# Optimization experiments

Hardware: AMD Instinct MI355X
Metric: run time of the kernel (lower is better)

The kernel has to match this reference:

```python
import jax, jax.numpy as jnp
import numpy as np

B, N, NF, H = 16, 128, 128, 128


def setup_inputs() -> dict:
    key = jax.random.key(0)
    ks = jax.random.split(key, 10)
    s = lambda k, sh: jax.random.normal(k, sh, dtype=jnp.float32) * (1.0 / np.sqrt(sh[0]))
    return {
        "node_feat": jax.random.normal(ks[0], (B, N, NF), dtype=jnp.float32),
        "pos": jax.random.normal(ks[1], (B, N, 3), dtype=jnp.float32),
        "valid": jnp.ones((B, N), dtype=jnp.float32),
        "adj": jax.random.uniform(ks[2], (B, N, N), dtype=jnp.float32),
        "We1": s(ks[3], (2 * NF + 2, H)),
        "We2": s(ks[4], (H, H)),
        "Wc1": s(ks[5], (H, H)),
        "Wc2": s(ks[6], (H, 1)),
        "Wn1": s(ks[7], (NF + H, H)),
        "Wn2": s(ks[8], (H, NF)),
        "Wi": s(ks[9], (H, 1)),
    }


def reference(node_feat, pos, valid, adj, We1, We2, Wc1, Wc2, Wn1, Wn2, Wi):
    silu = jax.nn.silu
    n = node_feat.shape[1]
    # all-pairs broadcast features [B,N,N,NF]
    hi = jnp.broadcast_to(node_feat[:, :, None, :], (B, n, n, NF))
    hj = jnp.broadcast_to(node_feat[:, None, :, :], (B, n, n, NF))
    vec = pos[:, :, None, :] - pos[:, None, :, :]            # [B,N,N,3]
    dist = jnp.sum(vec * vec, axis=-1, keepdims=True)        # [B,N,N,1]
    adj4 = adj[..., None]                                    # [B,N,N,1]
    edge_input = jnp.concatenate([hi, hj, dist, adj4], axis=-1)
    m_ij = silu(silu(edge_input @ We1) @ We2)                # [B,N,N,H]
    # normalized direction vectors
    norm = jnp.linalg.norm(vec, axis=-1, keepdims=True)
    vecn = vec / jnp.maximum(norm, 1e-10)
    # pairwise valid mask [B,N,N,1]
    vmask = (valid[:, :, None] * valid[:, None, :])[..., None]
    # coordinate update
    C = (1.0 / (jnp.sum(valid, axis=-1) - 1.0))[:, None, None]
    phi_x = silu(m_ij @ Wc1) @ Wc2                           # [B,N,N,1]
    pos_new = pos + C * jnp.sum(vecn * phi_x * vmask, axis=2)
    # inference gating
    e_ij = jax.nn.sigmoid(m_ij @ Wi)
    m_ij = m_ij * e_ij
    # masked message aggregation over j
    message = jnp.sum(m_ij * adj4, axis=2)                   # [B,N,H]
    node_input = jnp.concatenate([node_feat, message], axis=-1)
    node_new = node_feat + silu(node_input @ Wn1) @ Wn2
    return node_new, pos_new
```

## Files before the change

kernel.cpp:

```cpp
#include <hip/hip_runtime.h>
#include <hip/hip_bf16.h>

#define B_  16
#define N_  128
#define NF_ 128
#define H_  128

typedef __attribute__((ext_vector_type(8))) short short8;
typedef __attribute__((ext_vector_type(4))) float floatx4;

__device__ __forceinline__ float silu_f(float x) {
    return x * __builtin_amdgcn_rcpf(1.0f + __expf(-x));
}
__device__ __forceinline__ float sigm_f(float x) {
    return __builtin_amdgcn_rcpf(1.0f + __expf(-x));
}
__device__ __forceinline__ unsigned short f2bf(float x) {
    union { float f; unsigned u; } v; v.f = x;
    unsigned r = (v.u + 0x7FFFu + ((v.u >> 16) & 1u)) >> 16;
    return (unsigned short)r;
}
__device__ __forceinline__ short f2bf_fast(float x) {
    union { __hip_bfloat16 h; short s; } u;
    u.h = __float2bfloat16(x);
    return u.s;
}
__device__ __forceinline__ float bf2f(unsigned short s) {
    union { unsigned u; float f; } v; v.u = ((unsigned)s) << 16;
    return v.f;
}
__device__ __forceinline__ int swz(int row, int k) {
    return row * 256 + ((((k >> 3) ^ (row & 15)) << 4) | ((k & 7) << 1));
}

__global__ __launch_bounds__(128) void k1_pre(const float* __restrict__ nf,
                                              const float* __restrict__ We1,
                                              float* __restrict__ A_ws,
                                              float* __restrict__ Bm_ws) {
    const int b  = blockIdx.x >> 4;
    const int r0 = (blockIdx.x & 15) << 3;
    const int h  = threadIdx.x;
    __shared__ float rows[8][128];
#pragma unroll
    for (int r = 0; r < 8; ++r)
        rows[r][h] = nf[((size_t)(b * N_ + r0 + r)) * NF_ + h];
    __syncthreads();
    float a[8], bm[8];
#pragma unroll
    for (int r = 0; r < 8; ++r) { a[r] = 0.f; bm[r] = 0.f; }
    for (int c = 0; c < NF_; ++c) {
        const float w1 = We1[c * H_ + h];
        const float w2 = We1[(NF_ + c) * H_ + h];
#pragma unroll
        for (int r = 0; r < 8; ++r) {
            const float x = rows[r][c];
            a[r]  = fmaf(x, w1, a[r]);
            bm[r] = fmaf(x, w2, bm[r]);
        }
    }
#pragma unroll
    for (int r = 0; r < 8; ++r) {
        A_ws [((size_t)(b * N_ + r0 + r)) * H_ + h] = a[r];
        Bm_ws[((size_t)(b * N_ + r0 + r)) * H_ + h] = bm[r];
    }
}

__global__ __launch_bounds__(64) void kC(const float* __restrict__ valid,
                                         float* __restrict__ Cinv) {
    const int b = blockIdx.x;
    const int t = threadIdx.x;
    float v = valid[b * N_ + t] + valid[b * N_ + 64 + t];
#pragma unroll
    for (int m = 32; m >= 1; m >>= 1) v += __shfl_down(v, m, 64);
    if (t == 0) Cinv[b] = 1.0f / (v - 1.0f);
}

#define OFF_BM    0
#define OFF_W2T   32768
#define OFF_WC1X  65536
#define OFF_MB    102400
#define OFF_AW    135168
#define OFF_WAB   139264
#define OFF_WC2   140288
#define OFF_POSJ  140800
#define OFF_VALJ  142336
#define OFF_POSI  142848
#define OFF_VALI  142976
#define SMEM_K2   143040

__global__ __launch_bounds__(512, 2) void k2_edge(
        const float* __restrict__ pos,
        const float* __restrict__ valid,
        const float* __restrict__ adj,
        const float* __restrict__ We1,
        const float* __restrict__ We2,
        const float* __restrict__ Wc1,
        const float* __restrict__ Wc2,
        const float* __restrict__ Wi,
        const float* __restrict__ A_ws,
        const float* __restrict__ Bm_ws,
        const float* __restrict__ Cinv,
        float* __restrict__ msg_ws,
        float* __restrict__ pos_out) {
    __shared__ __align__(16) char smem[SMEM_K2];
    char* BMb   = smem + OFF_BM;
    char* W2Tb  = smem + OFF_W2T;
    char* WC1Xb = smem + OFF_WC1X;
    char* MBb   = smem + OFF_MB;
    float* AWf  = (float*)(smem + OFF_AW);
    float* WABf = (float*)(smem + OFF_WAB);
    float* wc2s = (float*)(smem + OFF_WC2);
    float* posj = (float*)(smem + OFF_POSJ);
    float* valj = (float*)(smem + OFF_VALJ);
    float* posi = (float*)(smem + OFF_POSI);
    float* vali = (float*)(smem + OFF_VALI);

    const int tid = threadIdx.x;
    const int b   = blockIdx.x >> 4;
    const int i0  = (blockIdx.x & 15) << 3;

    for (int q = tid; q < (N_ * H_) / 4; q += 512) {
        const int j  = q >> 5;
        const int ch = (q << 2) & 127;
        const float4 v = *(const float4*)(Bm_ws + ((size_t)(b * N_ + j)) * H_ + ch);
        ushort4 o;
        o.x = f2bf(v.x); o.y = f2bf(v.y); o.z = f2bf(v.z); o.w = f2bf(v.w);
        *(ushort4*)(BMb + swz(j, ch)) = o;
    }
    for (int x = tid; x < H_ * H_; x += 512) {
        const int k = x >> 7, n = x & 127;
        *(unsigned short*)(W2Tb + swz(n, k)) = f2bf(We2[x]);
    }
    for (int x = tid; x < H_ * H_; x += 512) {
        const int k = x >> 7, n = x & 127;
        *(unsigned short*)(WC1Xb + swz(n, k)) = f2bf(Wc1[x]);
    }
    if (tid < 128)
        *(unsigned short*)(WC1Xb + swz(128, tid)) = f2bf(Wi[tid]);
    for (int x = tid; x < 15 * 128; x += 512)
        ((unsigned short*)(WC1Xb + 129 * 256))[x] = 0;
    for (int x = tid; x < 8 * H_; x += 512)
        AWf[x] = A_ws[((size_t)(b * N_ + i0)) * H_ + x];
    if (tid < 256) WABf[tid] = We1[256 * H_ + tid];
    if (tid < 128) {
        wc2s[tid] = Wc2[tid];
        valj[tid] = valid[b * N_ + tid];
    }
    if (tid >= 128) posj[tid - 128] = pos[b * N_ * 3 + (tid - 128)];
    if (tid < 24)   posi[tid] = pos[b * N_ * 3 + i0 * 3 + tid];
    if (tid >= 32 && tid < 40) vali[tid - 32] = valid[b * N_ + i0 + (tid - 32)];
    __syncthreads();

    const int w  = tid >> 6;
    const int l  = tid & 63;
    const int lr = l & 15;
    const int lg = l >> 4;
    const int i  = i0 + w;
    char* MBw = MBb + w * 4096;

    int csx[4];
#pragma unroll
    for (int ks = 0; ks < 4; ++ks) csx[ks] = ((ks * 4 + lg) ^ lr) << 4;

    float wc2v[8];
#pragma unroll
    for (int nt = 0; nt < 8; ++nt) wc2v[nt] = wc2s[nt * 16 + lr];
    const float vi   = vali[w];
    const float pix  = posi[w * 3 + 0], piy = posi[w * 3 + 1], piz = posi[w * 3 + 2];
    const float cinv = Cinv[b];

    float msg[8] = {0.f, 0.f, 0.f, 0.f, 0.f, 0.f, 0.f, 0.f};
    float px = 0.f, py = 0.f, pz = 0.f;
    const floatx4 zf = {0.f, 0.f, 0.f, 0.f};

    for (int jp = 0; jp < 4; ++jp) {
        const int j0 = jp * 32;
        float adjv[2], vmv[2], dst[2], vnx[2], vny[2], vnz[2];
#pragma unroll
        for (int c = 0; c < 2; ++c) {
            const int jj = j0 + c * 16 + lr;
            adjv[c] = adj[((size_t)(b * N_ + i)) * N_ + jj];
            const float vj = valj[jj];
            const float vx = pix - posj[jj * 3 + 0];
            const float vy = piy - posj[jj * 3 + 1];
            const float vz = piz - posj[jj * 3 + 2];
            dst[c] = vx * vx + vy * vy + vz * vz;
            vmv[c] = vi * vj;
            const float rn = __builtin_amdgcn_rcpf(fmaxf(sqrtf(dst[c]), 1e-10f));
            vnx[c] = vx * rn; vny[c] = vy * rn; vnz[c] = vz * rn;
        }

        short8 af[2][4];
#pragma unroll
        for (int c = 0; c < 2; ++c) {
            const int jj = j0 + c * 16 + lr;
#pragma unroll
            for (int ks = 0; ks < 4; ++ks) {
                const int co = ks * 32 + lg * 8;
                const short8 bm8 = *(const short8*)(BMb + jj * 256 + csx[ks]);
                const floatx4 a0 = *(const floatx4*)(AWf + w * 128 + co);
                const floatx4 a1 = *(const floatx4*)(AWf + w * 128 + co + 4);
                const floatx4 wa0 = *(const floatx4*)(WABf + co);
                const floatx4 wa1 = *(const floatx4*)(WABf + co + 4);
                const floatx4 wb0 = *(const floatx4*)(WABf + 128 + co);
                const floatx4 wb1 = *(const floatx4*)(WABf + 128 + co + 4);
#pragma unroll
                for (int e = 0; e < 8; ++e) {
                    const float aw = (e < 4) ? a0[e & 3] : a1[e & 3];
                    const float wa = (e < 4) ? wa0[e & 3] : wa1[e & 3];
                    const float wb = (e < 4) ? wb0[e & 3] : wb1[e & 3];
                    const float pre = aw + bf2f((unsigned short)bm8[e])
                                    + dst[c] * wa + adjv[c] * wb;
                    af[c][ks][e] = f2bf_fast(silu_f(pre));
                }
            }
        }

        floatx4 acc1[2][8];
#pragma unroll
        for (int c = 0; c < 2; ++c)
#pragma unroll
            for (int nt = 0; nt < 8; ++nt) acc1[c][nt] = zf;
#pragma unroll
        for (int nt = 0; nt < 8; ++nt)
#pragma unroll
            for (int ks = 0; ks < 4; ++ks) {
                const short8 bf = *(const short8*)(W2Tb + (nt * 16 + lr) * 256 + csx[ks]);
                acc1[0][nt] = __builtin_amdgcn_mfma_f32_16x16x32_bf16(af[0][ks], bf, acc1[0][nt], 0, 0, 0);
                acc1[1][nt] = __builtin_amdgcn_mfma_f32_16x16x32_bf16(af[1][ks], bf, acc1[1][nt], 0, 0, 0);
            }
#pragma unroll
        for (int c = 0; c < 2; ++c)
#pragma unroll
            for (int nt = 0; nt < 8; ++nt)
#pragma unroll
                for (int r = 0; r < 4; ++r)
                    acc1[c][nt][r] = silu_f(acc1[c][nt][r]);

        short8 af2[2][4];
#pragma unroll
        for (int c = 0; c < 2; ++c) {
#pragma unroll
            for (int nt = 0; nt < 8; ++nt)
#pragma unroll
                for (int r = 0; r < 4; ++r)
                    *(unsigned short*)(MBw + swz(lg * 4 + r, nt * 16 + lr)) =
                        (unsigned short)f2bf_fast(acc1[c][nt][r]);
#pragma unroll
            for (int ks = 0; ks < 4; ++ks)
                af2[c][ks] = *(const short8*)(MBw + lr * 256 + csx[ks]);
        }

        floatx4 accg[2];
        accg[0] = zf; accg[1] = zf;
#pragma unroll
        for (int ks = 0; ks < 4; ++ks) {
            const short8 bf = *(const short8*)(WC1Xb + (128 + lr) * 256 + csx[ks]);
            accg[0] = __builtin_amdgcn_mfma_f32_16x16x32_bf16(af2[0][ks], bf, accg[0], 0, 0, 0);
            accg[1] = __builtin_amdgcn_mfma_f32_16x16x32_bf16(af2[1][ks], bf, accg[1], 0, 0, 0);
        }
#pragma unroll
        for (int c = 0; c < 2; ++c) {
            float t4[4];
#pragma unroll
            for (int r = 0; r < 4; ++r) {
                const float ep  = __shfl(accg[c][r], l & 48);
                const float ajr = __shfl(adjv[c], (l & 48) | (lg * 4 + r));
                t4[r] = sigm_f(ep) * ajr;
            }
#pragma unroll
            for (int nt = 0; nt < 8; ++nt)
                msg[nt] += acc1[c][nt][0] * t4[0] + acc1[c][nt][1] * t4[1]
                         + acc1[c][nt][2] * t4[2] + acc1[c][nt][3] * t4[3];
        }

        float ph[2][4] = {{0.f, 0.f, 0.f, 0.f}, {0.f, 0.f, 0.f, 0.f}};
#pragma unroll
        for (int nt = 0; nt < 8; ++nt) {
            floatx4 acc2a = zf, acc2b = zf;
#pragma unroll
            for (int ks = 0; ks < 4; ++ks) {
                const short8 bf = *(const short8*)(WC1Xb + (nt * 16 + lr) * 256 + csx[ks]);
                acc2a = __builtin_amdgcn_mfma_f32_16x16x32_bf16(af2[0][ks], bf, acc2a, 0, 0, 0);
                acc2b = __builtin_amdgcn_mfma_f32_16x16x32_bf16(af2[1][ks], bf, acc2b, 0, 0, 0);
            }
            const float wv = wc2v[nt];
#pragma unroll
            for (int r = 0; r < 4; ++r) {
                ph[0][r] = fmaf(silu_f(acc2a[r]), wv, ph[0][r]);
                ph[1][r] = fmaf(silu_f(acc2b[r]), wv, ph[1][r]);
            }
        }
#pragma unroll
        for (int msk = 1; msk <= 8; msk <<= 1)
#pragma unroll
            for (int c = 0; c < 2; ++c)
#pragma unroll
                for (int r = 0; r < 4; ++r)
                    ph[c][r] += __shfl_xor(ph[c][r], msk);
        const int src = ((lr >> 2) << 4) | lr;
        const int rr  = lr & 3;
#pragma unroll
        for (int c = 0; c < 2; ++c) {
            const float q0 = __shfl(ph[c][0], src), q1 = __shfl(ph[c][1], src);
            const float q2 = __shfl(ph[c][2], src), q3 = __shfl(ph[c][3], src);
            const float phl = rr == 0 ? q0 : rr == 1 ? q1 : rr == 2 ? q2 : q3;
            const float pm = phl * vmv[c];
            px = fmaf(vnx[c], pm, px); py = fmaf(vny[c], pm, py); pz = fmaf(vnz[c], pm, pz);
        }
    }

#pragma unroll
    for (int msk = 16; msk <= 32; msk <<= 1)
#pragma unroll
        for (int nt = 0; nt < 8; ++nt)
            msg[nt] += __shfl_xor(msg[nt], msk);
    if (l < 16) {
#pragma unroll
        for (int nt = 0; nt < 8; ++nt)
            msg_ws[((size_t)(b * N_ + i)) * H_ + nt * 16 + l] = msg[nt];
    }
#pragma unroll
    for (int msk = 1; msk <= 8; msk <<= 1) {
        px += __shfl_xor(px, msk);
        py += __shfl_xor(py, msk);
        pz += __shfl_xor(pz, msk);
    }
    if (l == 0) {
        const size_t o = ((size_t)(b * N_ + i)) * 3;
        pos_out[o + 0] = pos[o + 0] + cinv * px;
        pos_out[o + 1] = pos[o + 1] + cinv * py;
        pos_out[o + 2] = pos[o + 2] + cinv * pz;
    }
}

__global__ __launch_bounds__(128) void k3_node(
        const float* __restrict__ nf,
        const float* __restrict__ Wn1,
        const float* __restrict__ Wn2,
        const float* __restrict__ msg_ws,
        float* __restrict__ out) {
    const int b  = blockIdx.x >> 4;
    const int r0 = (blockIdx.x & 15) << 3;
    const int h  = threadIdx.x;
    __shared__ float in_s[8][256];
    __shared__ float t_s[8][128];
#pragma unroll
    for (int r = 0; r < 8; ++r) {
        in_s[r][h]       = nf[((size_t)(b * N_ + r0 + r)) * NF_ + h];
        in_s[r][128 + h] = msg_ws[((size_t)(b * N_ + r0 + r)) * H_ + h];
    }
    __syncthreads();
    float acc[8];
#pragma unroll
    for (int r = 0; r < 8; ++r) acc[r] = 0.f;
    for (int c = 0; c < 256; ++c) {
        const float wv = Wn1[c * H_ + h];
#pragma unroll
        for (int r = 0; r < 8; ++r) acc[r] = fmaf(in_s[r][c], wv, acc[r]);
    }
#pragma unroll
    for (int r = 0; r < 8; ++r) t_s[r][h] = silu_f(acc[r]);
    __syncthreads();
    float o[8];
#pragma unroll
    for (int r = 0; r < 8; ++r) o[r] = 0.f;
    for (int c = 0; c < 128; ++c) {
        const float wv = Wn2[c * NF_ + h];
#pragma unroll
        for (int r = 0; r < 8; ++r) o[r] = fmaf(t_s[r][c], wv, o[r]);
    }
#pragma unroll
    for (int r = 0; r < 8; ++r)
        out[((size_t)(b * N_ + r0 + r)) * NF_ + h] = in_s[r][h] + o[r];
}

extern "C" void kernel_launch(void* const* d_in, const int* in_sizes, int n_in,
                              void* d_out, int out_size, void* d_ws, size_t ws_size,
                              hipStream_t stream) {
    const float* node_feat = (const float*)d_in[0];
    const float* pos   = (const float*)d_in[1];
    const float* valid = (const float*)d_in[2];
    const float* adj   = (const float*)d_in[3];
    const float* We1   = (const float*)d_in[4];
    const float* We2   = (const float*)d_in[5];
    const float* Wc1   = (const float*)d_in[6];
    const float* Wc2   = (const float*)d_in[7];
    const float* Wn1   = (const float*)d_in[8];
    const float* Wn2   = (const float*)d_in[9];
    const float* Wi    = (const float*)d_in[10];

    float* out     = (float*)d_out;
    float* pos_out = out + (size_t)B_ * N_ * NF_;

    const size_t node_elems = (size_t)B_ * N_ * H_;
    if (ws_size < (3 * node_elems + B_) * sizeof(float)) return;
    float* A_ws   = (float*)d_ws;
    float* Bm_ws  = A_ws + node_elems;
    float* msg_ws = Bm_ws + node_elems;
    float* Cinv   = msg_ws + node_elems;

    k1_pre<<<B_ * 16, 128, 0, stream>>>(node_feat, We1, A_ws, Bm_ws);
    kC<<<B_, 64, 0, stream>>>(valid, Cinv);
    k2_edge<<<B_ * 16, 512, 0, stream>>>(pos, valid, adj, We1, We2, Wc1, Wc2, Wi,
                                         A_ws, Bm_ws, Cinv, msg_ws, pos_out);
    k3_node<<<B_ * 16, 128, 0, stream>>>(node_feat, Wn1, Wn2, msg_ws, out);
}
```

Before: 78.92 us.

## Transpose edge MFMA output to feed next GEMM from registers, drop LDS staging

The first edge GEMM now computes the transposed product, with weights as the A operand. Its silu'd accumulator fragments can then be converted to bf16 and used directly as B operands of 16x16x16 bf16 MFMAs for the gating and coordinate GEMMs. This removes the per-wave LDS write/read round trip for the intermediate m_ij tile and about 32KB of shared memory. The epilogue reductions for the gate, phi and message are reworked to match the transposed layout. In exchange it issues twice as many smaller-K MFMAs, and relies on the 16x16x16 instruction being available, with an inline asm fallback otherwise.

```diff
diff --git a/kernel.cpp b/kernel.cpp
--- a/kernel.cpp
+++ b/kernel.cpp
@@ -7,6 +7,7 @@
 #define H_  128
 
 typedef __attribute__((ext_vector_type(8))) short short8;
+typedef __attribute__((ext_vector_type(4))) short short4v;
 typedef __attribute__((ext_vector_type(4))) float floatx4;
 
 __device__ __forceinline__ float silu_f(float x) {
@@ -32,6 +33,18 @@
 __device__ __forceinline__ int swz(int row, int k) {
     return row * 256 + ((((k >> 3) ^ (row & 15)) << 4) | ((k & 7) << 1));
 }
+
+#if defined(__has_builtin) && __has_builtin(__builtin_amdgcn_mfma_f32_16x16x16bf16_1k)
+#define MFMA16(a, b, c) __builtin_amdgcn_mfma_f32_16x16x16bf16_1k(a, b, c, 0, 0, 0)
+#else
+__device__ __forceinline__ floatx4 mfma16_asm(short4v a, short4v b, floatx4 c) {
+    floatx4 d;
+    asm volatile("v_mfma_f32_16x16x16_bf16 %0, %1, %2, %3"
+                 : "=v"(d) : "v"(a), "v"(b), "v"(c));
+    return d;
+}
+#define MFMA16(a, b, c) mfma16_asm(a, b, c)
+#endif
 
 __global__ __launch_bounds__(128) void k1_pre(const float* __restrict__ nf,
                                               const float* __restrict__ We1,
@@ -78,15 +91,14 @@
 #define OFF_BM    0
 #define OFF_W2T   32768
 #define OFF_WC1X  65536
-#define OFF_MB    102400
-#define OFF_AW    135168
-#define OFF_WAB   139264
-#define OFF_WC2   140288
-#define OFF_POSJ  140800
-#define OFF_VALJ  142336
-#define OFF_POSI  142848
-#define OFF_VALI  142976
-#define SMEM_K2   143040
+#define OFF_AW    102400
+#define OFF_WAB   106496
+#define OFF_WC2   107520
+#define OFF_POSJ  108032
+#define OFF_VALJ  109568
+#define OFF_POSI  110080
+#define OFF_VALI  110208
+#define SMEM_K2   110272
 
 __global__ __launch_bounds__(512, 2) void k2_edge(
         const float* __restrict__ pos,
@@ -106,7 +118,6 @@
     char* BMb   = smem + OFF_BM;
     char* W2Tb  = smem + OFF_W2T;
     char* WC1Xb = smem + OFF_WC1X;
-    char* MBb   = smem + OFF_MB;
     float* AWf  = (float*)(smem + OFF_AW);
     float* WABf = (float*)(smem + OFF_WAB);
     float* wc2s = (float*)(smem + OFF_WC2);
@@ -156,22 +167,24 @@
     const int lr = l & 15;
     const int lg = l >> 4;
     const int i  = i0 + w;
-    char* MBw = MBb + w * 4096;
 
     int csx[4];
 #pragma unroll
     for (int ks = 0; ks < 4; ++ks) csx[ks] = ((ks * 4 + lg) ^ lr) << 4;
-
-    float wc2v[8];
-#pragma unroll
-    for (int nt = 0; nt < 8; ++nt) wc2v[nt] = wc2s[nt * 16 + lr];
+    int cs16[8];
+#pragma unroll
+    for (int ks = 0; ks < 8; ++ks)
+        cs16[ks] = ((((2 * ks + (lg >> 1)) ^ lr) << 4) | ((lg & 1) << 3));
+
     const float vi   = vali[w];
     const float pix  = posi[w * 3 + 0], piy = posi[w * 3 + 1], piz = posi[w * 3 + 2];
     const float cinv = Cinv[b];
 
-    float msg[8] = {0.f, 0.f, 0.f, 0.f, 0.f, 0.f, 0.f, 0.f};
+    floatx4 msgv[8];
+    const floatx4 zf = {0.f, 0.f, 0.f, 0.f};
+#pragma unroll
+    for (int nt = 0; nt < 8; ++nt) msgv[nt] = zf;
     float px = 0.f, py = 0.f, pz = 0.f;
-    const floatx4 zf = {0.f, 0.f, 0.f, 0.f};
 
     for (int jp = 0; jp < 4; ++jp) {
         const int j0 = jp * 32;
@@ -226,8 +239,8 @@
 #pragma unroll
             for (int ks = 0; ks < 4; ++ks) {
                 const short8 bf = *(const short8*)(W2Tb + (nt * 16 + lr) * 256 + csx[ks]);
-                acc1[0][nt] = __builtin_amdgcn_mfma_f32_16x16x32_bf16(af[0][ks], bf, acc1[0][nt], 0, 0, 0);
-                acc1[1][nt] = __builtin_amdgcn_mfma_f32_16x16x32_bf16(af[1][ks], bf, acc1[1][nt], 0, 0, 0);
+                acc1[0][nt] = __builtin_amdgcn_mfma_f32_16x16x32_bf16(bf, af[0][ks], acc1[0][nt], 0, 0, 0);
+                acc1[1][nt] = __builtin_amdgcn_mfma_f32_16x16x32_bf16(bf, af[1][ks], acc1[1][nt], 0, 0, 0);
             }
 #pragma unroll
         for (int c = 0; c < 2; ++c)
@@ -237,88 +250,73 @@
                 for (int r = 0; r < 4; ++r)
                     acc1[c][nt][r] = silu_f(acc1[c][nt][r]);
 
-        short8 af2[2][4];
-#pragma unroll
-        for (int c = 0; c < 2; ++c) {
-#pragma unroll
-            for (int nt = 0; nt < 8; ++nt)
-#pragma unroll
-                for (int r = 0; r < 4; ++r)
-                    *(unsigned short*)(MBw + swz(lg * 4 + r, nt * 16 + lr)) =
-                        (unsigned short)f2bf_fast(acc1[c][nt][r]);
-#pragma unroll
-            for (int ks = 0; ks < 4; ++ks)
-                af2[c][ks] = *(const short8*)(MBw + lr * 256 + csx[ks]);
-        }
+        short4v af2[2][8];
+#pragma unroll
+        for (int c = 0; c < 2; ++c)
+#pragma unroll
+            for (int ks = 0; ks < 8; ++ks) {
+                short4v t;
+                t[0] = f2bf_fast(acc1[c][ks][0]);
+                t[1] = f2bf_fast(acc1[c][ks][1]);
+                t[2] = f2bf_fast(acc1[c][ks][2]);
+                t[3] = f2bf_fast(acc1[c][ks][3]);
+                af2[c][ks] = t;
+            }
 
         floatx4 accg[2];
         accg[0] = zf; accg[1] = zf;
 #pragma unroll
-        for (int ks = 0; ks < 4; ++ks) {
-            const short8 bf = *(const short8*)(WC1Xb + (128 + lr) * 256 + csx[ks]);
-            accg[0] = __builtin_amdgcn_mfma_f32_16x16x32_bf16(af2[0][ks], bf, accg[0], 0, 0, 0);
-            accg[1] = __builtin_amdgcn_mfma_f32_16x16x32_bf16(af2[1][ks], bf, accg[1], 0, 0, 0);
+        for (int ks = 0; ks < 8; ++ks) {
+            const short4v ga = *(const short4v*)(WC1Xb + (128 + lr) * 256 + cs16[ks]);
+            accg[0] = MFMA16(ga, af2[0][ks], accg[0]);
+            accg[1] = MFMA16(ga, af2[1][ks], accg[1]);
         }
 #pragma unroll
         for (int c = 0; c < 2; ++c) {
-            float t4[4];
-#pragma unroll
-            for (int r = 0; r < 4; ++r) {
-                const float ep  = __shfl(accg[c][r], l & 48);
-                const float ajr = __shfl(adjv[c], (l & 48) | (lg * 4 + r));
-                t4[r] = sigm_f(ep) * ajr;
-            }
+            const float ep = __shfl(accg[c][0], lr);
+            const float t  = sigm_f(ep) * adjv[c];
 #pragma unroll
             for (int nt = 0; nt < 8; ++nt)
-                msg[nt] += acc1[c][nt][0] * t4[0] + acc1[c][nt][1] * t4[1]
-                         + acc1[c][nt][2] * t4[2] + acc1[c][nt][3] * t4[3];
-        }
-
-        float ph[2][4] = {{0.f, 0.f, 0.f, 0.f}, {0.f, 0.f, 0.f, 0.f}};
+                msgv[nt] += acc1[c][nt] * t;
+        }
+
+        float ph[2] = {0.f, 0.f};
 #pragma unroll
         for (int nt = 0; nt < 8; ++nt) {
             floatx4 acc2a = zf, acc2b = zf;
 #pragma unroll
-            for (int ks = 0; ks < 4; ++ks) {
-                const short8 bf = *(const short8*)(WC1Xb + (nt * 16 + lr) * 256 + csx[ks]);
-                acc2a = __builtin_amdgcn_mfma_f32_16x16x32_bf16(af2[0][ks], bf, acc2a, 0, 0, 0);
-                acc2b = __builtin_amdgcn_mfma_f32_16x16x32_bf16(af2[1][ks], bf, acc2b, 0, 0, 0);
+            for (int ks = 0; ks < 8; ++ks) {
+                const short4v wf = *(const short4v*)(WC1Xb + (nt * 16 + lr) * 256 + cs16[ks]);
+                acc2a = MFMA16(wf, af2[0][ks], acc2a);
+                acc2b = MFMA16(wf, af2[1][ks], acc2b);
             }
-            const float wv = wc2v[nt];
+            const floatx4 wv4 = *(const floatx4*)(wc2s + nt * 16 + 4 * lg);
 #pragma unroll
             for (int r = 0; r < 4; ++r) {
-                ph[0][r] = fmaf(silu_f(acc2a[r]), wv, ph[0][r]);
-                ph[1][r] = fmaf(silu_f(acc2b[r]), wv, ph[1][r]);
+                ph[0] = fmaf(silu_f(acc2a[r]), wv4[r], ph[0]);
+                ph[1] = fmaf(silu_f(acc2b[r]), wv4[r], ph[1]);
             }
         }
 #pragma unroll
-        for (int msk = 1; msk <= 8; msk <<= 1)
-#pragma unroll
-            for (int c = 0; c < 2; ++c)
-#pragma unroll
-                for (int r = 0; r < 4; ++r)
-                    ph[c][r] += __shfl_xor(ph[c][r], msk);
-        const int src = ((lr >> 2) << 4) | lr;
-        const int rr  = lr & 3;
-#pragma unroll
         for (int c = 0; c < 2; ++c) {
-            const float q0 = __shfl(ph[c][0], src), q1 = __shfl(ph[c][1], src);
-            const float q2 = __shfl(ph[c][2], src), q3 = __shfl(ph[c][3], src);
-            const float phl = rr == 0 ? q0 : rr == 1 ? q1 : rr == 2 ? q2 : q3;
-            const float pm = phl * vmv[c];
+            ph[c] += __shfl_xor(ph[c], 16);
+            ph[c] += __shfl_xor(ph[c], 32);
+            const float pm = ph[c] * vmv[c];
             px = fmaf(vnx[c], pm, px); py = fmaf(vny[c], pm, py); pz = fmaf(vnz[c], pm, pz);
         }
     }
 
 #pragma unroll
-    for (int msk = 16; msk <= 32; msk <<= 1)
+    for (int msk = 1; msk <= 8; msk <<= 1)
 #pragma unroll
         for (int nt = 0; nt < 8; ++nt)
-            msg[nt] += __shfl_xor(msg[nt], msk);
-    if (l < 16) {
+#pragma unroll
+            for (int r = 0; r < 4; ++r)
+                msgv[nt][r] += __shfl_xor(msgv[nt][r], msk);
+    if (lr == 0) {
 #pragma unroll
         for (int nt = 0; nt < 8; ++nt)
-            msg_ws[((size_t)(b * N_ + i)) * H_ + nt * 16 + l] = msg[nt];
+            *(floatx4*)(msg_ws + ((size_t)(b * N_ + i)) * H_ + nt * 16 + 4 * lg) = msgv[nt];
     }
 #pragma unroll
     for (int msk = 1; msk <= 8; msk <<= 1) {
```

New measurement: 193.6 us. 145% more time.
